# Optimization experiments

Measured on AMD Instinct MI355X. Metric: run time of the kernel, lower is better.

The kernel has to match this reference:

```python
import jax, jax.numpy as jnp
import numpy as np

N = 100000   # nodes
E = 1600000  # edges
F_IN = 64    # input features
H = 64       # hidden channels
C = 40       # classes


def setup_inputs() -> dict:
    key = jax.random.key(0)
    k1, k2, k3, k4 = jax.random.split(key, 4)
    x = jax.random.normal(k1, (N, F_IN), dtype=jnp.float32)
    edge_index = jax.random.randint(k2, (2, E), 0, N, dtype=jnp.int64)
    W1 = jax.random.normal(k3, (F_IN, H), dtype=jnp.float32) / np.sqrt(F_IN)
    b1 = jnp.zeros((H,), dtype=jnp.float32)
    W2 = jax.random.normal(k4, (H, C), dtype=jnp.float32) / np.sqrt(H)
    b2 = jnp.zeros((C,), dtype=jnp.float32)
    return {"x": x, "edge_index": edge_index, "W1": W1, "b1": b1, "W2": W2, "b2": b2}


def gcn_conv(x, src, dst, W, b):
    """PyG-style GCNConv: self-loops + symmetric deg^{-1/2} normalization.
    src/dst already include self-loops. x: [N, Fin], W: [Fin, Fout]."""
    n = x.shape[0]
    deg = jax.ops.segment_sum(jnp.ones_like(dst, dtype=x.dtype), dst, num_segments=n)
    dinv = jnp.where(deg > 0, jax.lax.rsqrt(deg), jnp.zeros_like(deg))
    norm = dinv[src] * dinv[dst]          # [E+N]
    h = x @ W                             # transform first (Fin -> Fout)
    msg = h[src] * norm[:, None]          # gather + scale, [E+N, Fout]
    out = jax.ops.segment_sum(msg, dst, num_segments=n)  # scatter-add
    return out + b


def reference(x, edge_index, W1, b1, W2, b2):
    n = x.shape[0]
    loops = jnp.arange(n, dtype=edge_index.dtype)
    src = jnp.concatenate([edge_index[0], loops])
    dst = jnp.concatenate([edge_index[1], loops])
    h = jax.nn.relu(gcn_conv(x, src, dst, W1, b1))
    # F.dropout in eval mode (training=False) is identity
    out = gcn_conv(h, src, dst, W2, b2)
    return jax.nn.log_softmax(out, axis=1)
```

## Files before the change

### kernel.cpp

```cpp
#include <hip/hip_runtime.h>
#include <math.h>

#define F1 64
#define F2 40
#define NB 1024
#define TILE 4096
#define FCAP 3200

typedef unsigned int uint;

__device__ inline unsigned short f2bf(float f) {
    unsigned u = __float_as_uint(f);
    unsigned r = (u + 0x7FFFu + ((u >> 16) & 1u)) >> 16;
    return (unsigned short)r;
}
__device__ inline uint packbf(float lo, float hi) {
    return (uint)f2bf(lo) | ((uint)f2bf(hi) << 16);
}
__device__ inline float bf_lo(uint u) { return __uint_as_float(u << 16); }
__device__ inline float bf_hi(uint u) { return __uint_as_float(u & 0xFFFF0000u); }

__global__ __launch_bounds__(256) void k_bhist(const int* __restrict__ dst,
                                               int* __restrict__ bcnt, int e, int bsh) {
    __shared__ int h[NB];
    int tid = threadIdx.x;
    for (int i = tid; i < NB; i += 256) h[i] = 0;
    __syncthreads();
    int base = blockIdx.x * TILE;
    int lim = min(base + TILE, e);
    for (int i = base + tid; i < lim; i += 256) atomicAdd(&h[dst[i] >> bsh], 1);
    __syncthreads();
    for (int i = tid; i < NB; i += 256) if (h[i]) atomicAdd(&bcnt[i], h[i]);
}

__global__ __launch_bounds__(NB) void k_bscan(const int* __restrict__ bcnt,
                                              int* __restrict__ bptr, int* __restrict__ gcur,
                                              int* __restrict__ row_ptr, int n, int e) {
    __shared__ int sh[NB];
    int t = threadIdx.x;
    sh[t] = bcnt[t];
    __syncthreads();
    for (int off = 1; off < NB; off <<= 1) {
        int v = (t >= off) ? sh[t - off] : 0;
        __syncthreads();
        sh[t] += v;
        __syncthreads();
    }
    int ex = t ? sh[t - 1] : 0;
    bptr[t] = ex;
    gcur[t] = ex;
    if (t == NB - 1) bptr[NB] = sh[NB - 1];
    if (t == 0) row_ptr[n] = e;
}

__global__ __launch_bounds__(256) void k_bscatter(const int* __restrict__ src,
                                                  const int* __restrict__ dst,
                                                  int* gcur,
                                                  unsigned long long* __restrict__ pairs,
                                                  int e, int bsh) {
    __shared__ int lhist[NB];
    __shared__ int lstart[NB];
    __shared__ int delta[NB];
    __shared__ unsigned long long stage[TILE];
    int tid = threadIdx.x;
    for (int i = tid; i < NB; i += 256) lhist[i] = 0;
    __syncthreads();
    int base = blockIdx.x * TILE;
    int cnt = min(TILE, e - base);
    int sA[16], dA[16], rA[16];
#pragma unroll
    for (int k = 0; k < 16; ++k) {
        int i = base + k * 256 + tid;
        if (i < e) {
            sA[k] = src[i];
            dA[k] = dst[i];
            rA[k] = atomicAdd(&lhist[dA[k] >> bsh], 1);
        }
    }
    __syncthreads();
    if (tid < 64) {
        const int per = NB / 64;
        int v[per];
        int b0 = tid * per, s = 0;
#pragma unroll
        for (int j = 0; j < per; ++j) { v[j] = lhist[b0 + j]; s += v[j]; }
        int sc = s;
        for (int o = 1; o < 64; o <<= 1) { int u = __shfl_up(sc, o); if (tid >= o) sc += u; }
        int ex = sc - s;
#pragma unroll
        for (int j = 0; j < per; ++j) { lstart[b0 + j] = ex; ex += v[j]; }
    }
    __syncthreads();
    for (int i = tid; i < NB; i += 256) {
        int c = lhist[i];
        if (c) delta[i] = atomicAdd(&gcur[i], c) - lstart[i];
    }
    __syncthreads();
#pragma unroll
    for (int k = 0; k < 16; ++k) {
        int i = base + k * 256 + tid;
        if (i < e) {
            int b = dA[k] >> bsh;
            stage[lstart[b] + rA[k]] =
                ((unsigned long long)(unsigned)sA[k] << 32) | (unsigned)dA[k];
        }
    }
    __syncthreads();
    for (int p = tid; p < cnt; p += 256) {
        unsigned long long pr = stage[p];
        int b = ((int)(unsigned)pr) >> bsh;
        pairs[delta[b] + p] = pr;
    }
}

__global__ __launch_bounds__(256) void k_final(const unsigned long long* __restrict__ pairs,
                                               const int* __restrict__ bptr,
                                               int* __restrict__ srcs,
                                               int* __restrict__ row_ptr,
                                               float* __restrict__ dinv,
                                               int n, int bsh) {
    __shared__ int ldeg[128];
    __shared__ int lrow[128];
    __shared__ int lcur[128];
    __shared__ unsigned long long stg[FCAP];
    int b = blockIdx.x, tid = threadIdx.x;
    int beg = bptr[b], cnt = bptr[b + 1] - beg;
    int node0 = b << bsh;
    int bnodes = 1 << bsh;
    for (int i = tid; i < bnodes; i += 256) { ldeg[i] = 0; lcur[i] = 0; }
    bool fit = cnt <= FCAP;
    __syncthreads();
    if (fit) {
        for (int p = tid; p < cnt; p += 256) {
            unsigned long long pr = pairs[beg + p];
            stg[p] = pr;
            atomicAdd(&ldeg[((int)(unsigned)pr) - node0], 1);
        }
    } else {
        for (int p = tid; p < cnt; p += 256)
            atomicAdd(&ldeg[((int)(unsigned)pairs[beg + p]) - node0], 1);
    }
    __syncthreads();
    if (tid < 64) {
        int per = bnodes >> 6;
        int b0 = tid * per, s = 0;
        for (int j = 0; j < per; ++j) s += ldeg[b0 + j];
        int sc = s;
        for (int o = 1; o < 64; o <<= 1) { int u = __shfl_up(sc, o); if (tid >= o) sc += u; }
        int ex = sc - s;
        for (int j = 0; j < per; ++j) { lrow[b0 + j] = ex; ex += ldeg[b0 + j]; }
    }
    __syncthreads();
    for (int i = tid; i < bnodes; i += 256) {
        int node = node0 + i;
        if (node < n) {
            row_ptr[node] = beg + lrow[i];
            dinv[node] = rsqrtf((float)(ldeg[i] + 1));
        }
    }
    if (fit) {
        for (int p = tid; p < cnt; p += 256) {
            unsigned long long pr = stg[p];
            int dl = ((int)(unsigned)pr) - node0;
            int r = atomicAdd(&lcur[dl], 1);
            srcs[beg + lrow[dl] + r] = (int)(pr >> 32);
        }
    } else {
        for (int p = tid; p < cnt; p += 256) {
            unsigned long long pr = pairs[beg + p];
            int dl = ((int)(unsigned)pr) - node0;
            int r = atomicAdd(&lcur[dl], 1);
            srcs[beg + lrow[dl] + r] = (int)(pr >> 32);
        }
    }
}

__global__ __launch_bounds__(256) void k_gemm1(const float* __restrict__ x,
                                               const float* __restrict__ W,
                                               const float* __restrict__ dinv,
                                               unsigned short* __restrict__ h, int n,
                                               int nwaves) {
    int wid = blockIdx.x * 4 + (threadIdx.x >> 6);
    int lane = threadIdx.x & 63;
    float wcol[64];
#pragma unroll
    for (int k = 0; k < 64; ++k)
        wcol[k] = W[k * 64 + lane];
    for (int node = wid; node < n; node += nwaves) {
        int node_u = __builtin_amdgcn_readfirstlane(node);
        const float* arow = x + (size_t)node_u * 64;
        float acc = 0.0f;
#pragma unroll
        for (int k4 = 0; k4 < 16; ++k4) {
            float4 a = *(const float4*)(arow + k4 * 4);
            acc = fmaf(a.x, wcol[k4 * 4 + 0], acc);
            acc = fmaf(a.y, wcol[k4 * 4 + 1], acc);
            acc = fmaf(a.z, wcol[k4 * 4 + 2], acc);
            acc = fmaf(a.w, wcol[k4 * 4 + 3], acc);
        }
        h[(size_t)node_u * 64 + lane] = f2bf(acc * dinv[node_u]);
    }
}

__global__ __launch_bounds__(256) void k_gather(const uint4* __restrict__ h4,
                                                const int* __restrict__ srcs,
                                                const int* __restrict__ row_ptr,
                                                const float* __restrict__ dinv,
                                                const float* __restrict__ b,
                                                uint4* __restrict__ aggb, int n) {
    int node = (int)(((long long)blockIdx.x * 256 + threadIdx.x) >> 5);
    int l32 = threadIdx.x & 31;
    if (node >= n) return;
    int slot = l32 >> 3, j = l32 & 7;
    float a0x=0,a0y=0,a1x=0,a1y=0,a2x=0,a2y=0,a3x=0,a3y=0;
    if (slot == 0) {
        uint4 u = h4[(size_t)node * 8 + j];
        a0x = bf_lo(u.x); a0y = bf_hi(u.x);
        a1x = bf_lo(u.y); a1y = bf_hi(u.y);
        a2x = bf_lo(u.z); a2y = bf_hi(u.z);
        a3x = bf_lo(u.w); a3y = bf_hi(u.w);
    }
    int e0 = row_ptr[node], cnt = row_ptr[node + 1] - e0;
    int p = slot;
    for (; p + 4 < cnt; p += 8) {
        int s0 = srcs[e0 + p], s1 = srcs[e0 + p + 4];
        uint4 u0 = h4[(size_t)s0 * 8 + j];
        uint4 u1 = h4[(size_t)s1 * 8 + j];
        a0x += bf_lo(u0.x) + bf_lo(u1.x);  a0y += bf_hi(u0.x) + bf_hi(u1.x);
        a1x += bf_lo(u0.y) + bf_lo(u1.y);  a1y += bf_hi(u0.y) + bf_hi(u1.y);
        a2x += bf_lo(u0.z) + bf_lo(u1.z);  a2y += bf_hi(u0.z) + bf_hi(u1.z);
        a3x += bf_lo(u0.w) + bf_lo(u1.w);  a3y += bf_hi(u0.w) + bf_hi(u1.w);
    }
    for (; p < cnt; p += 4) {
        int s0 = srcs[e0 + p];
        uint4 u0 = h4[(size_t)s0 * 8 + j];
        a0x += bf_lo(u0.x);  a0y += bf_hi(u0.x);
        a1x += bf_lo(u0.y);  a1y += bf_hi(u0.y);
        a2x += bf_lo(u0.z);  a2y += bf_hi(u0.z);
        a3x += bf_lo(u0.w);  a3y += bf_hi(u0.w);
    }
#define COMB(o) \
    a0x += __shfl_xor(a0x, o); a0y += __shfl_xor(a0y, o); \
    a1x += __shfl_xor(a1x, o); a1y += __shfl_xor(a1y, o); \
    a2x += __shfl_xor(a2x, o); a2y += __shfl_xor(a2y, o); \
    a3x += __shfl_xor(a3x, o); a3y += __shfl_xor(a3y, o);
    COMB(8) COMB(16)
#undef COMB
    if (slot == 0) {
        float di = dinv[node];
        float4 bl = *(const float4*)&b[8 * j];
        float4 bh = *(const float4*)&b[8 * j + 4];
        float v0 = fmaxf(fmaf(a0x, di, bl.x), 0.0f);
        float v1 = fmaxf(fmaf(a0y, di, bl.y), 0.0f);
        float v2 = fmaxf(fmaf(a1x, di, bl.z), 0.0f);
        float v3 = fmaxf(fmaf(a1y, di, bl.w), 0.0f);
        float v4 = fmaxf(fmaf(a2x, di, bh.x), 0.0f);
        float v5 = fmaxf(fmaf(a2y, di, bh.y), 0.0f);
        float v6 = fmaxf(fmaf(a3x, di, bh.z), 0.0f);
        float v7 = fmaxf(fmaf(a3y, di, bh.w), 0.0f);
        uint4 r;
        r.x = packbf(v0, v1); r.y = packbf(v2, v3);
        r.z = packbf(v4, v5); r.w = packbf(v6, v7);
        aggb[(size_t)node * 8 + j] = r;
    }
}

__global__ __launch_bounds__(256) void k_trans2(const uint* __restrict__ aggu,
                                                const float* __restrict__ W2,
                                                const float* __restrict__ dinv,
                                                unsigned short* __restrict__ t, int n,
                                                int nwaves) {
    int wid = blockIdx.x * 4 + (threadIdx.x >> 6);
    int lane = threadIdx.x & 63;
    float wcol[64];
#pragma unroll
    for (int k = 0; k < 64; ++k)
        wcol[k] = (lane < 40) ? W2[k * 40 + lane] : 0.0f;
    for (int node = wid; node < n; node += nwaves) {
        int node_u = __builtin_amdgcn_readfirstlane(node);
        const uint* arow = aggu + (size_t)node_u * 32;
        float acc = 0.0f;
#pragma unroll
        for (int k4 = 0; k4 < 8; ++k4) {
            uint4 a = *(const uint4*)(arow + k4 * 4);
            acc = fmaf(bf_lo(a.x), wcol[8 * k4 + 0], acc);
            acc = fmaf(bf_hi(a.x), wcol[8 * k4 + 1], acc);
            acc = fmaf(bf_lo(a.y), wcol[8 * k4 + 2], acc);
            acc = fmaf(bf_hi(a.y), wcol[8 * k4 + 3], acc);
            acc = fmaf(bf_lo(a.z), wcol[8 * k4 + 4], acc);
            acc = fmaf(bf_hi(a.z), wcol[8 * k4 + 5], acc);
            acc = fmaf(bf_lo(a.w), wcol[8 * k4 + 6], acc);
            acc = fmaf(bf_hi(a.w), wcol[8 * k4 + 7], acc);
        }
        float di = dinv[node_u];
        if (lane < 40) t[(size_t)node_u * 40 + lane] = f2bf(acc * di);
    }
}

__global__ __launch_bounds__(256) void k_gather40(const uint2* __restrict__ t2,
                                                  const int* __restrict__ srcs,
                                                  const int* __restrict__ row_ptr,
                                                  const float* __restrict__ dinv,
                                                  const float* __restrict__ b2,
                                                  float* __restrict__ out, int n) {
    int node = (int)(((long long)blockIdx.x * 256 + threadIdx.x) >> 5);
    int lane = threadIdx.x & 63;
    int l32 = lane & 31;
    if (node >= n) return;
    int slot = l32 / 10;
    int j = l32 - slot * 10;
    bool act = slot < 3;
    float a0=0, a1=0, a2=0, a3=0;
    if (slot == 0) {
        uint2 u = t2[(size_t)node * 10 + j];
        a0 = bf_lo(u.x); a1 = bf_hi(u.x);
        a2 = bf_lo(u.y); a3 = bf_hi(u.y);
    }
    int e0 = row_ptr[node];
    int cnt = act ? (row_ptr[node + 1] - e0) : 0;
    int p = slot;
    for (; p + 3 < cnt; p += 6) {
        int s0 = srcs[e0 + p], s1 = srcs[e0 + p + 3];
        uint2 u0 = t2[(size_t)s0 * 10 + j];
        uint2 u1 = t2[(size_t)s1 * 10 + j];
        a0 += bf_lo(u0.x) + bf_lo(u1.x);  a1 += bf_hi(u0.x) + bf_hi(u1.x);
        a2 += bf_lo(u0.y) + bf_lo(u1.y);  a3 += bf_hi(u0.y) + bf_hi(u1.y);
    }
    for (; p < cnt; p += 3) {
        int s0 = srcs[e0 + p];
        uint2 u0 = t2[(size_t)s0 * 10 + j];
        a0 += bf_lo(u0.x);  a1 += bf_hi(u0.x);
        a2 += bf_lo(u0.y);  a3 += bf_hi(u0.y);
    }
    float t0 = a0 + __shfl(a0, lane + 10) + __shfl(a0, lane + 20);
    float t1 = a1 + __shfl(a1, lane + 10) + __shfl(a1, lane + 20);
    float t2s = a2 + __shfl(a2, lane + 10) + __shfl(a2, lane + 20);
    float t3 = a3 + __shfl(a3, lane + 10) + __shfl(a3, lane + 20);
    bool actc = l32 < 10;
    float di = dinv[node];
    float4 bb = actc ? *(const float4*)&b2[4 * l32] : make_float4(0, 0, 0, 0);
    float v0 = fmaf(t0, di, bb.x);
    float v1 = fmaf(t1, di, bb.y);
    float v2 = fmaf(t2s, di, bb.z);
    float v3 = fmaf(t3, di, bb.w);
    float mv = actc ? fmaxf(fmaxf(v0, v1), fmaxf(v2, v3)) : -INFINITY;
    for (int o = 16; o; o >>= 1) mv = fmaxf(mv, __shfl_xor(mv, o));
    float ex = actc ? (expf(v0 - mv) + expf(v1 - mv) + expf(v2 - mv) + expf(v3 - mv)) : 0.0f;
    float s = ex;
    for (int o = 16; o; o >>= 1) s += __shfl_xor(s, o);
    float ls = mv + logf(s);
    if (actc) {
        float4 r = make_float4(v0 - ls, v1 - ls, v2 - ls, v3 - ls);
        *(float4*)&out[(size_t)node * 40 + 4 * l32] = r;
    }
}

extern "C" void kernel_launch(void* const* d_in, const int* in_sizes, int n_in,
                              void* d_out, int out_size, void* d_ws, size_t ws_size,
                              hipStream_t stream) {
    const float* x  = (const float*)d_in[0];
    const int*   ei = (const int*)d_in[1];
    const float* W1 = (const float*)d_in[2];
    const float* b1 = (const float*)d_in[3];
    const float* W2 = (const float*)d_in[4];
    const float* b2 = (const float*)d_in[5];

    const int N = in_sizes[0] / F1;
    const int E = in_sizes[1] / 2;
    const int* src = ei;
    const int* dst = ei + E;

    int bsh = 7;
    while ((((N - 1) >> bsh) + 1) > NB) ++bsh;
    const int NBu = ((N - 1) >> bsh) + 1;

    uint4* h1b     = (uint4*)d_ws;
    uint4* aggb    = h1b + (size_t)N * 8;
    uint2* tb      = (uint2*)(aggb + (size_t)N * 8);
    unsigned long long* pairs = (unsigned long long*)(tb + (size_t)N * 10);
    int*   srcs    = (int*)(pairs + E);
    int*   row_ptr = srcs + E;
    float* dinv    = (float*)(row_ptr + N + 1);
    int*   bcnt    = (int*)(dinv + N);
    int*   bptr    = bcnt + NB;
    int*   gcur    = bptr + NB + 1;
    float* outp    = (float*)d_out;

    const int B = 256;
    const int GT = (E + TILE - 1) / TILE;

    hipMemsetAsync(bcnt, 0, NB * sizeof(int), stream);
    k_bhist<<<GT, B, 0, stream>>>(dst, bcnt, E, bsh);
    k_bscan<<<1, NB, 0, stream>>>(bcnt, bptr, gcur, row_ptr, N, E);
    k_bscatter<<<GT, B, 0, stream>>>(src, dst, gcur, pairs, E, bsh);
    k_final<<<NBu, B, 0, stream>>>(pairs, bptr, srcs, row_ptr, dinv, N, bsh);

    const int TB = 2048;
    k_gemm1<<<TB, B, 0, stream>>>(x, W1, dinv, (unsigned short*)h1b, N, TB * 4);
    k_gather<<<(N + 7) / 8, B, 0, stream>>>(h1b, srcs, row_ptr, dinv, b1, aggb, N);

    k_trans2<<<TB, B, 0, stream>>>((const uint*)aggb, W2, dinv, (unsigned short*)tb, N, TB * 4);
    k_gather40<<<(N + 7) / 8, B, 0, stream>>>(tb, srcs, row_ptr, dinv, b2, outp, N);
}
```

Measured before the change: 282.4 us.

## Restructure dense transforms to one node per lane with register-blocked outputs

Both dense transform kernels (x@W1 and agg@W2) switch from one-node-per-wave with per-lane weight columns to one-node-per-lane, each lane computing half the output columns in 32 or 20 register accumulators. Weight rows become wave-uniform broadcast loads, and each lane reads its own input row with vector loads. Outputs are packed to bf16 and written as wide vector stores. This is meant to raise arithmetic reuse and cut the per-node serialization of the old grid-stride loop. The cost is more register pressure and uncoalesced per-lane row reads, since lanes are 256 B or 64 B apart.

```diff
diff --git a/kernel.cpp b/kernel.cpp
--- a/kernel.cpp
+++ b/kernel.cpp
@@ -178,27 +178,45 @@
 __global__ __launch_bounds__(256) void k_gemm1(const float* __restrict__ x,
                                                const float* __restrict__ W,
                                                const float* __restrict__ dinv,
-                                               unsigned short* __restrict__ h, int n,
-                                               int nwaves) {
+                                               unsigned short* __restrict__ h, int n) {
     int wid = blockIdx.x * 4 + (threadIdx.x >> 6);
     int lane = threadIdx.x & 63;
-    float wcol[64];
-#pragma unroll
-    for (int k = 0; k < 64; ++k)
-        wcol[k] = W[k * 64 + lane];
-    for (int node = wid; node < n; node += nwaves) {
-        int node_u = __builtin_amdgcn_readfirstlane(node);
-        const float* arow = x + (size_t)node_u * 64;
-        float acc = 0.0f;
-#pragma unroll
-        for (int k4 = 0; k4 < 16; ++k4) {
-            float4 a = *(const float4*)(arow + k4 * 4);
-            acc = fmaf(a.x, wcol[k4 * 4 + 0], acc);
-            acc = fmaf(a.y, wcol[k4 * 4 + 1], acc);
-            acc = fmaf(a.z, wcol[k4 * 4 + 2], acc);
-            acc = fmaf(a.w, wcol[k4 * 4 + 3], acc);
-        }
-        h[(size_t)node_u * 64 + lane] = f2bf(acc * dinv[node_u]);
+    int half = wid & 1;
+    int node0 = (wid >> 1) * 64;
+    if (node0 >= n) return;
+    int node = node0 + lane;
+    int nc = min(node, n - 1);
+    const float* arow = x + (size_t)nc * 64;
+    float di = dinv[nc];
+    float acc[32];
+#pragma unroll
+    for (int c = 0; c < 32; ++c) acc[c] = 0.0f;
+    const float* wb = W + half * 32;
+#pragma unroll 4
+    for (int k4 = 0; k4 < 16; ++k4) {
+        float4 a = *(const float4*)(arow + k4 * 4);
+#pragma unroll
+        for (int r = 0; r < 4; ++r) {
+            float xv = (r == 0) ? a.x : (r == 1) ? a.y : (r == 2) ? a.z : a.w;
+            const float4* wr = (const float4*)(wb + (k4 * 4 + r) * 64);
+#pragma unroll
+            for (int c4 = 0; c4 < 8; ++c4) {
+                float4 wv = wr[c4];
+                acc[c4 * 4 + 0] = fmaf(xv, wv.x, acc[c4 * 4 + 0]);
+                acc[c4 * 4 + 1] = fmaf(xv, wv.y, acc[c4 * 4 + 1]);
+                acc[c4 * 4 + 2] = fmaf(xv, wv.z, acc[c4 * 4 + 2]);
+                acc[c4 * 4 + 3] = fmaf(xv, wv.w, acc[c4 * 4 + 3]);
+            }
+        }
+    }
+    if (node < n) {
+        uint us[16];
+#pragma unroll
+        for (int c2 = 0; c2 < 16; ++c2)
+            us[c2] = packbf(acc[2 * c2] * di, acc[2 * c2 + 1] * di);
+        uint4* hp = (uint4*)(h + (size_t)node * 64 + half * 32);
+#pragma unroll
+        for (int q = 0; q < 4; ++q) hp[q] = ((const uint4*)us)[q];
     }
 }
 
@@ -268,32 +286,50 @@
 __global__ __launch_bounds__(256) void k_trans2(const uint* __restrict__ aggu,
                                                 const float* __restrict__ W2,
                                                 const float* __restrict__ dinv,
-                                                unsigned short* __restrict__ t, int n,
-                                                int nwaves) {
+                                                unsigned short* __restrict__ t, int n) {
     int wid = blockIdx.x * 4 + (threadIdx.x >> 6);
     int lane = threadIdx.x & 63;
-    float wcol[64];
-#pragma unroll
-    for (int k = 0; k < 64; ++k)
-        wcol[k] = (lane < 40) ? W2[k * 40 + lane] : 0.0f;
-    for (int node = wid; node < n; node += nwaves) {
-        int node_u = __builtin_amdgcn_readfirstlane(node);
-        const uint* arow = aggu + (size_t)node_u * 32;
-        float acc = 0.0f;
-#pragma unroll
-        for (int k4 = 0; k4 < 8; ++k4) {
-            uint4 a = *(const uint4*)(arow + k4 * 4);
-            acc = fmaf(bf_lo(a.x), wcol[8 * k4 + 0], acc);
-            acc = fmaf(bf_hi(a.x), wcol[8 * k4 + 1], acc);
-            acc = fmaf(bf_lo(a.y), wcol[8 * k4 + 2], acc);
-            acc = fmaf(bf_hi(a.y), wcol[8 * k4 + 3], acc);
-            acc = fmaf(bf_lo(a.z), wcol[8 * k4 + 4], acc);
-            acc = fmaf(bf_hi(a.z), wcol[8 * k4 + 5], acc);
-            acc = fmaf(bf_lo(a.w), wcol[8 * k4 + 6], acc);
-            acc = fmaf(bf_hi(a.w), wcol[8 * k4 + 7], acc);
-        }
-        float di = dinv[node_u];
-        if (lane < 40) t[(size_t)node_u * 40 + lane] = f2bf(acc * di);
+    int half = wid & 1;
+    int node0 = (wid >> 1) * 64;
+    if (node0 >= n) return;
+    int node = node0 + lane;
+    int nc = min(node, n - 1);
+    const uint* arow = aggu + (size_t)nc * 32;
+    float di = dinv[nc];
+    float acc[20];
+#pragma unroll
+    for (int c = 0; c < 20; ++c) acc[c] = 0.0f;
+    const float* wb = W2 + half * 20;
+#pragma unroll 2
+    for (int k8 = 0; k8 < 8; ++k8) {
+        uint4 a = *(const uint4*)(arow + k8 * 4);
+        float xs0 = bf_lo(a.x), xs1 = bf_hi(a.x);
+        float xs2 = bf_lo(a.y), xs3 = bf_hi(a.y);
+        float xs4 = bf_lo(a.z), xs5 = bf_hi(a.z);
+        float xs6 = bf_lo(a.w), xs7 = bf_hi(a.w);
+#pragma unroll
+        for (int r = 0; r < 8; ++r) {
+            float xv = (r == 0) ? xs0 : (r == 1) ? xs1 : (r == 2) ? xs2 : (r == 3) ? xs3
+                     : (r == 4) ? xs4 : (r == 5) ? xs5 : (r == 6) ? xs6 : xs7;
+            const float4* wr = (const float4*)(wb + (k8 * 8 + r) * 40);
+#pragma unroll
+            for (int c4 = 0; c4 < 5; ++c4) {
+                float4 wv = wr[c4];
+                acc[c4 * 4 + 0] = fmaf(xv, wv.x, acc[c4 * 4 + 0]);
+                acc[c4 * 4 + 1] = fmaf(xv, wv.y, acc[c4 * 4 + 1]);
+                acc[c4 * 4 + 2] = fmaf(xv, wv.z, acc[c4 * 4 + 2]);
+                acc[c4 * 4 + 3] = fmaf(xv, wv.w, acc[c4 * 4 + 3]);
+            }
+        }
+    }
+    if (node < n) {
+        uint us[10];
+#pragma unroll
+        for (int c2 = 0; c2 < 10; ++c2)
+            us[c2] = packbf(acc[2 * c2] * di, acc[2 * c2 + 1] * di);
+        uint2* tp = (uint2*)(t + (size_t)node * 40 + half * 20);
+#pragma unroll
+        for (int q = 0; q < 5; ++q) tp[q] = ((const uint2*)us)[q];
     }
 }
 
@@ -395,10 +431,11 @@
     k_bscatter<<<GT, B, 0, stream>>>(src, dst, gcur, pairs, E, bsh);
     k_final<<<NBu, B, 0, stream>>>(pairs, bptr, srcs, row_ptr, dinv, N, bsh);
 
-    const int TB = 2048;
-    k_gemm1<<<TB, B, 0, stream>>>(x, W1, dinv, (unsigned short*)h1b, N, TB * 4);
+    const int GW = (2 * ((N + 63) / 64) + 3) / 4;
+
+    k_gemm1<<<GW, B, 0, stream>>>(x, W1, dinv, (unsigned short*)h1b, N);
     k_gather<<<(N + 7) / 8, B, 0, stream>>>(h1b, srcs, row_ptr, dinv, b1, aggb, N);
 
-    k_trans2<<<TB, B, 0, stream>>>((const uint*)aggb, W2, dinv, (unsigned short*)tb, N, TB * 4);
+    k_trans2<<<GW, B, 0, stream>>>((const uint*)aggb, W2, dinv, (unsigned short*)tb, N);
     k_gather40<<<(N + 7) / 8, B, 0, stream>>>(tb, srcs, row_ptr, dinv, b2, outp, N);
 }
```

New measurement: 330.0 us. 16.9% more time.

## Use bf16x3 MFMA for both dense feature transforms with prepacked weights

Applied to the files above, without the earlier changes.

Replaces the per-lane scalar FMA GEMMs in k_gemm1 and k_trans2 with 16x16x32 bf16 MFMA tiles. Inputs and weights are split into high and low bf16 parts to keep near-fp32 accuracy. A new k_wprep kernel packs W1 and W2 into the MFMA operand layout once per call. This targets the ALU and register cost of the dense transforms, at the price of an extra launch, extra MFMAs for the split terms, and scattered 2-byte output stores.

```diff
diff --git a/kernel.cpp b/kernel.cpp
--- a/kernel.cpp
+++ b/kernel.cpp
@@ -8,6 +8,10 @@
 #define FCAP 3200
 
 typedef unsigned int uint;
+typedef __attribute__((ext_vector_type(8))) short s8v;
+typedef __attribute__((ext_vector_type(4))) float f4v;
+
+union U8 { s8v s; uint4 q; uint u[4]; };
 
 __device__ inline unsigned short f2bf(float f) {
     unsigned u = __float_as_uint(f);
@@ -19,6 +23,14 @@
 }
 __device__ inline float bf_lo(uint u) { return __uint_as_float(u << 16); }
 __device__ inline float bf_hi(uint u) { return __uint_as_float(u & 0xFFFF0000u); }
+
+__device__ inline void split2(float a, float b, uint* hu, uint* lu) {
+    unsigned short ha = f2bf(a), hb = f2bf(b);
+    *hu = (uint)ha | ((uint)hb << 16);
+    float ra = a - __uint_as_float((uint)ha << 16);
+    float rb = b - __uint_as_float((uint)hb << 16);
+    *lu = packbf(ra, rb);
+}
 
 __global__ __launch_bounds__(256) void k_bhist(const int* __restrict__ dst,
                                                int* __restrict__ bcnt, int e, int bsh) {
@@ -175,31 +187,87 @@
     }
 }
 
+__global__ __launch_bounds__(256) void k_wprep(const float* __restrict__ W1,
+                                               const float* __restrict__ W2,
+                                               uint4* __restrict__ wf1,
+                                               uint4* __restrict__ wf2) {
+    int g = blockIdx.x * 256 + threadIdx.x;
+    if (g < 512) {
+        int ks = g >> 8, ct = (g >> 6) & 3, l = g & 63;
+        int c = 16 * ct + (l & 15);
+        int kb = 32 * ks + 8 * (l >> 4);
+        uint hu[4], lu[4];
+#pragma unroll
+        for (int i = 0; i < 4; ++i)
+            split2(W1[(kb + 2 * i) * 64 + c], W1[(kb + 2 * i + 1) * 64 + c], &hu[i], &lu[i]);
+        wf1[(size_t)(ks * 4 + ct) * 64 + l]       = make_uint4(hu[0], hu[1], hu[2], hu[3]);
+        wf1[(size_t)((2 + ks) * 4 + ct) * 64 + l] = make_uint4(lu[0], lu[1], lu[2], lu[3]);
+    } else if (g < 896) {
+        int v = g - 512;
+        int ks = v / 192, rem = v % 192;
+        int ct = rem >> 6, l = rem & 63;
+        int c = 16 * ct + (l & 15);
+        int kb = 32 * ks + 8 * (l >> 4);
+        uint hu[4], lu[4];
+#pragma unroll
+        for (int i = 0; i < 4; ++i) {
+            float a = (c < 40) ? W2[(kb + 2 * i) * 40 + c] : 0.0f;
+            float b = (c < 40) ? W2[(kb + 2 * i + 1) * 40 + c] : 0.0f;
+            split2(a, b, &hu[i], &lu[i]);
+        }
+        wf2[(size_t)(ks * 3 + ct) * 64 + l]       = make_uint4(hu[0], hu[1], hu[2], hu[3]);
+        wf2[(size_t)((2 + ks) * 3 + ct) * 64 + l] = make_uint4(lu[0], lu[1], lu[2], lu[3]);
+    }
+}
+
 __global__ __launch_bounds__(256) void k_gemm1(const float* __restrict__ x,
-                                               const float* __restrict__ W,
+                                               const uint4* __restrict__ wf1,
                                                const float* __restrict__ dinv,
-                                               unsigned short* __restrict__ h, int n,
-                                               int nwaves) {
-    int wid = blockIdx.x * 4 + (threadIdx.x >> 6);
-    int lane = threadIdx.x & 63;
-    float wcol[64];
-#pragma unroll
-    for (int k = 0; k < 64; ++k)
-        wcol[k] = W[k * 64 + lane];
-    for (int node = wid; node < n; node += nwaves) {
-        int node_u = __builtin_amdgcn_readfirstlane(node);
-        const float* arow = x + (size_t)node_u * 64;
-        float acc = 0.0f;
-#pragma unroll
-        for (int k4 = 0; k4 < 16; ++k4) {
-            float4 a = *(const float4*)(arow + k4 * 4);
-            acc = fmaf(a.x, wcol[k4 * 4 + 0], acc);
-            acc = fmaf(a.y, wcol[k4 * 4 + 1], acc);
-            acc = fmaf(a.z, wcol[k4 * 4 + 2], acc);
-            acc = fmaf(a.w, wcol[k4 * 4 + 3], acc);
-        }
-        h[(size_t)node_u * 64 + lane] = f2bf(acc * dinv[node_u]);
-    }
+                                               unsigned short* __restrict__ h, int n) {
+    int w = threadIdx.x >> 6, l = threadIdx.x & 63;
+    int node0 = blockIdx.x * 64 + w * 16;
+    int ar = min(node0 + (l & 15), n - 1);
+    const float* ap = x + (size_t)ar * 64 + 8 * (l >> 4);
+    float4 a0 = *(const float4*)ap;
+    float4 a1 = *(const float4*)(ap + 4);
+    float4 a2 = *(const float4*)(ap + 32);
+    float4 a3 = *(const float4*)(ap + 36);
+    U8 ah0, al0, ah1, al1;
+    split2(a0.x, a0.y, &ah0.u[0], &al0.u[0]);
+    split2(a0.z, a0.w, &ah0.u[1], &al0.u[1]);
+    split2(a1.x, a1.y, &ah0.u[2], &al0.u[2]);
+    split2(a1.z, a1.w, &ah0.u[3], &al0.u[3]);
+    split2(a2.x, a2.y, &ah1.u[0], &al1.u[0]);
+    split2(a2.z, a2.w, &ah1.u[1], &al1.u[1]);
+    split2(a3.x, a3.y, &ah1.u[2], &al1.u[2]);
+    split2(a3.z, a3.w, &ah1.u[3], &al1.u[3]);
+    f4v acc[4];
+#pragma unroll
+    for (int ct = 0; ct < 4; ++ct) acc[ct] = (f4v){0.0f, 0.0f, 0.0f, 0.0f};
+#pragma unroll
+    for (int ct = 0; ct < 4; ++ct) {
+        U8 bh0, bh1, bl0, bl1;
+        bh0.q = wf1[(size_t)(0 * 4 + ct) * 64 + l];
+        bh1.q = wf1[(size_t)(1 * 4 + ct) * 64 + l];
+        bl0.q = wf1[(size_t)(2 * 4 + ct) * 64 + l];
+        bl1.q = wf1[(size_t)(3 * 4 + ct) * 64 + l];
+        acc[ct] = __builtin_amdgcn_mfma_f32_16x16x32_bf16(ah0.s, bh0.s, acc[ct], 0, 0, 0);
+        acc[ct] = __builtin_amdgcn_mfma_f32_16x16x32_bf16(ah1.s, bh1.s, acc[ct], 0, 0, 0);
+        acc[ct] = __builtin_amdgcn_mfma_f32_16x16x32_bf16(al0.s, bh0.s, acc[ct], 0, 0, 0);
+        acc[ct] = __builtin_amdgcn_mfma_f32_16x16x32_bf16(al1.s, bh1.s, acc[ct], 0, 0, 0);
+        acc[ct] = __builtin_amdgcn_mfma_f32_16x16x32_bf16(ah0.s, bl0.s, acc[ct], 0, 0, 0);
+        acc[ct] = __builtin_amdgcn_mfma_f32_16x16x32_bf16(ah1.s, bl1.s, acc[ct], 0, 0, 0);
+    }
+    int r0 = node0 + (l >> 4) * 4;
+    float dv[4];
+#pragma unroll
+    for (int r = 0; r < 4; ++r) dv[r] = dinv[min(r0 + r, n - 1)];
+#pragma unroll
+    for (int ct = 0; ct < 4; ++ct)
+#pragma unroll
+        for (int r = 0; r < 4; ++r)
+            if (r0 + r < n)
+                h[(size_t)(r0 + r) * 64 + 16 * ct + (l & 15)] = f2bf(acc[ct][r] * dv[r]);
 }
 
 __global__ __launch_bounds__(256) void k_gather(const uint4* __restrict__ h4,
@@ -265,35 +333,42 @@
     }
 }
 
-__global__ __launch_bounds__(256) void k_trans2(const uint* __restrict__ aggu,
-                                                const float* __restrict__ W2,
+__global__ __launch_bounds__(256) void k_trans2(const uint4* __restrict__ aggb,
+                                                const uint4* __restrict__ wf2,
                                                 const float* __restrict__ dinv,
-                                                unsigned short* __restrict__ t, int n,
-                                                int nwaves) {
-    int wid = blockIdx.x * 4 + (threadIdx.x >> 6);
-    int lane = threadIdx.x & 63;
-    float wcol[64];
-#pragma unroll
-    for (int k = 0; k < 64; ++k)
-        wcol[k] = (lane < 40) ? W2[k * 40 + lane] : 0.0f;
-    for (int node = wid; node < n; node += nwaves) {
-        int node_u = __builtin_amdgcn_readfirstlane(node);
-        const uint* arow = aggu + (size_t)node_u * 32;
-        float acc = 0.0f;
-#pragma unroll
-        for (int k4 = 0; k4 < 8; ++k4) {
-            uint4 a = *(const uint4*)(arow + k4 * 4);
-            acc = fmaf(bf_lo(a.x), wcol[8 * k4 + 0], acc);
-            acc = fmaf(bf_hi(a.x), wcol[8 * k4 + 1], acc);
-            acc = fmaf(bf_lo(a.y), wcol[8 * k4 + 2], acc);
-            acc = fmaf(bf_hi(a.y), wcol[8 * k4 + 3], acc);
-            acc = fmaf(bf_lo(a.z), wcol[8 * k4 + 4], acc);
-            acc = fmaf(bf_hi(a.z), wcol[8 * k4 + 5], acc);
-            acc = fmaf(bf_lo(a.w), wcol[8 * k4 + 6], acc);
-            acc = fmaf(bf_hi(a.w), wcol[8 * k4 + 7], acc);
-        }
-        float di = dinv[node_u];
-        if (lane < 40) t[(size_t)node_u * 40 + lane] = f2bf(acc * di);
+                                                unsigned short* __restrict__ t, int n) {
+    int w = threadIdx.x >> 6, l = threadIdx.x & 63;
+    int node0 = blockIdx.x * 64 + w * 16;
+    int ar = min(node0 + (l & 15), n - 1);
+    U8 a0, a1;
+    a0.q = aggb[(size_t)ar * 8 + 0 + (l >> 4)];
+    a1.q = aggb[(size_t)ar * 8 + 4 + (l >> 4)];
+    f4v acc[3];
+#pragma unroll
+    for (int ct = 0; ct < 3; ++ct) acc[ct] = (f4v){0.0f, 0.0f, 0.0f, 0.0f};
+#pragma unroll
+    for (int ct = 0; ct < 3; ++ct) {
+        U8 bh0, bh1, bl0, bl1;
+        bh0.q = wf2[(size_t)(0 * 3 + ct) * 64 + l];
+        bh1.q = wf2[(size_t)(1 * 3 + ct) * 64 + l];
+        bl0.q = wf2[(size_t)(2 * 3 + ct) * 64 + l];
+        bl1.q = wf2[(size_t)(3 * 3 + ct) * 64 + l];
+        acc[ct] = __builtin_amdgcn_mfma_f32_16x16x32_bf16(a0.s, bh0.s, acc[ct], 0, 0, 0);
+        acc[ct] = __builtin_amdgcn_mfma_f32_16x16x32_bf16(a1.s, bh1.s, acc[ct], 0, 0, 0);
+        acc[ct] = __builtin_amdgcn_mfma_f32_16x16x32_bf16(a0.s, bl0.s, acc[ct], 0, 0, 0);
+        acc[ct] = __builtin_amdgcn_mfma_f32_16x16x32_bf16(a1.s, bl1.s, acc[ct], 0, 0, 0);
+    }
+    int r0 = node0 + (l >> 4) * 4;
+    float dv[4];
+#pragma unroll
+    for (int r = 0; r < 4; ++r) dv[r] = dinv[min(r0 + r, n - 1)];
+#pragma unroll
+    for (int ct = 0; ct < 3; ++ct) {
+        int col = 16 * ct + (l & 15);
+#pragma unroll
+        for (int r = 0; r < 4; ++r)
+            if (col < 40 && r0 + r < n)
+                t[(size_t)(r0 + r) * 40 + col] = f2bf(acc[ct][r] * dv[r]);
     }
 }
 
@@ -377,7 +452,9 @@
     uint4* h1b     = (uint4*)d_ws;
     uint4* aggb    = h1b + (size_t)N * 8;
     uint2* tb      = (uint2*)(aggb + (size_t)N * 8);
-    unsigned long long* pairs = (unsigned long long*)(tb + (size_t)N * 10);
+    uint4* wf1     = (uint4*)(tb + (size_t)N * 10);
+    uint4* wf2     = wf1 + 1024;
+    unsigned long long* pairs = (unsigned long long*)(wf2 + 768);
     int*   srcs    = (int*)(pairs + E);
     int*   row_ptr = srcs + E;
     float* dinv    = (float*)(row_ptr + N + 1);
@@ -389,16 +466,19 @@
     const int B = 256;
     const int GT = (E + TILE - 1) / TILE;
 
+    k_wprep<<<4, B, 0, stream>>>(W1, W2, wf1, wf2);
+
     hipMemsetAsync(bcnt, 0, NB * sizeof(int), stream);
     k_bhist<<<GT, B, 0, stream>>>(dst, bcnt, E, bsh);
     k_bscan<<<1, NB, 0, stream>>>(bcnt, bptr, gcur, row_ptr, N, E);
     k_bscatter<<<GT, B, 0, stream>>>(src, dst, gcur, pairs, E, bsh);
     k_final<<<NBu, B, 0, stream>>>(pairs, bptr, srcs, row_ptr, dinv, N, bsh);
 
-    const int TB = 2048;
-    k_gemm1<<<TB, B, 0, stream>>>(x, W1, dinv, (unsigned short*)h1b, N, TB * 4);
+    const int GM = (N + 63) / 64;
+
+    k_gemm1<<<GM, B, 0, stream>>>(x, wf1, dinv, (unsigned short*)h1b, N);
     k_gather<<<(N + 7) / 8, B, 0, stream>>>(h1b, srcs, row_ptr, dinv, b1, aggb, N);
 
-    k_trans2<<<TB, B, 0, stream>>>((const uint*)aggb, W2, dinv, (unsigned short*)tb, N, TB * 4);
+    k_trans2<<<GM, B, 0, stream>>>(aggb, wf2, dinv, (unsigned short*)tb, N);
     k_gather40<<<(N + 7) / 8, B, 0, stream>>>(tb, srcs, row_ptr, dinv, b2, outp, N);
 }
```

Measured after the change: 240.5 us. 14.8% less time.
